# Performance work log

Hardware: AMD Instinct MI355X
Metric: run time of the kernel (lower is better)

Reference implementation:

```python
import jax, jax.numpy as jnp
import numpy as np

LN_EPS = 1e-5      # torch.nn.LayerNorm default
NORM_EPS = 1e-12   # torch F.normalize default


def _layernorm(x, gamma, beta):
    mu = jnp.mean(x, axis=-1, keepdims=True)
    var = jnp.mean(jnp.square(x - mu), axis=-1, keepdims=True)
    return (x - mu) * jax.lax.rsqrt(var + LN_EPS) * gamma + beta


def _l2norm(x):
    # normalize over last (embedding) axis, matching F.normalize(dim=1) on [B,E,1,N]
    n = jnp.sqrt(jnp.sum(jnp.square(x), axis=-1, keepdims=True))
    return x / jnp.maximum(n, NORM_EPS)


def setup_inputs() -> dict:
    key = jax.random.key(0)
    ks = jax.random.split(key, 4)
    B, N, C, E = 8, 4096, 768, 768
    x = jax.random.normal(ks[0], (B, N, C), dtype=jnp.float32)
    w_qkv = jax.random.normal(ks[1], (C, 3 * E), dtype=jnp.float32) * (1.0 / np.sqrt(C))
    w_proj = jax.random.normal(ks[2], (E, C), dtype=jnp.float32) * (1.0 / np.sqrt(E))
    ln_in_g = jnp.ones((C,), jnp.float32)
    ln_in_b = jnp.zeros((C,), jnp.float32)
    ln_out_g = jnp.ones((E,), jnp.float32)
    ln_out_b = jnp.zeros((E,), jnp.float32)
    return {"x": x, "w_qkv": w_qkv, "w_proj": w_proj,
            "ln_in_g": ln_in_g, "ln_in_b": ln_in_b,
            "ln_out_g": ln_out_g, "ln_out_b": ln_out_b}


def reference(x, w_qkv, w_proj, ln_in_g, ln_in_b, ln_out_g, ln_out_b):
    # x: [B, N, C]
    h = _layernorm(x, ln_in_g, ln_in_b)
    qkv = h @ w_qkv                                  # [B, N, 3E]
    q, k, v = jnp.split(qkv, 3, axis=-1)             # each [B, N, E]
    phi_q = _l2norm(q)                               # per-token L2 over E
    phi_k = _l2norm(k)
    kv = jnp.sum(phi_k * v, axis=1)                  # [B, E] (sum over tokens N)
    attn = phi_q * kv[:, None, :]                    # [B, N, E]
    out = _layernorm(attn, ln_out_g, ln_out_b) @ w_proj  # [B, N, C]
    return out
```

## Files before the change

### kernel.cpp

```cpp
#include <hip/hip_runtime.h>
#include <hip/hip_bf16.h>
#include <cstdint>

typedef __bf16 bf16;
typedef __bf16 bf16x4 __attribute__((ext_vector_type(4)));
typedef __bf16 bf16x8 __attribute__((ext_vector_type(8)));
typedef float f32x4 __attribute__((ext_vector_type(4)));

#define GK 768
#define LN_EPS 1e-5f
#define NORM_EPS 1e-12f

__device__ __forceinline__ void gl_lds16(const void* g, void* l) {
  __builtin_amdgcn_global_load_lds(
      (__attribute__((address_space(1))) uint32_t*)(uintptr_t)g,
      (__attribute__((address_space(3))) uint32_t*)(uintptr_t)l,
      16, 0, 0);
}

__device__ __forceinline__ void blockReduce2w3(float& s, float& ss, float* sm) {
  #pragma unroll
  for (int o = 32; o > 0; o >>= 1) {
    s  += __shfl_down(s, o, 64);
    ss += __shfl_down(ss, o, 64);
  }
  int wave = threadIdx.x >> 6, lane = threadIdx.x & 63;
  if (lane == 0) { sm[wave] = s; sm[3 + wave] = ss; }
  __syncthreads();
  s  = sm[0] + sm[1] + sm[2];
  ss = sm[3] + sm[4] + sm[5];
  __syncthreads();
}

__global__ __launch_bounds__(256) void transpose_cvt(const float* __restrict__ w,
                                                     bf16* __restrict__ wt,
                                                     int R, int Ncols) {
  __shared__ float tile[32][33];
  int tx = threadIdx.x & 31, ty = threadIdx.x >> 5;
  int c0 = blockIdx.x * 32, r0 = blockIdx.y * 32;
  #pragma unroll
  for (int i = 0; i < 32; i += 8)
    tile[ty + i][tx] = w[(size_t)(r0 + ty + i) * Ncols + (c0 + tx)];
  __syncthreads();
  #pragma unroll
  for (int i = 0; i < 32; i += 8)
    wt[(size_t)(c0 + ty + i) * R + (r0 + tx)] = (bf16)tile[tx][ty + i];
}

__global__ __launch_bounds__(192) void ln_in_kernel(const float* __restrict__ x,
                                                    const float* __restrict__ g,
                                                    const float* __restrict__ b,
                                                    bf16* __restrict__ h) {
  __shared__ float sm[6];
  int row = blockIdx.x, t = threadIdx.x;
  const float* xr = x + (size_t)row * 768;
  float4 v = ((const float4*)xr)[t];
  float s  = v.x + v.y + v.z + v.w;
  float ss = v.x * v.x + v.y * v.y + v.z * v.z + v.w * v.w;
  blockReduce2w3(s, ss, sm);
  float mu  = s * (1.0f / 768.0f);
  float inv = rsqrtf(ss * (1.0f / 768.0f) - mu * mu + LN_EPS);
  float4 gg = ((const float4*)g)[t];
  float4 bb = ((const float4*)b)[t];
  bf16x4 o;
  o[0] = (bf16)((v.x - mu) * inv * gg.x + bb.x);
  o[1] = (bf16)((v.y - mu) * inv * gg.y + bb.y);
  o[2] = (bf16)((v.z - mu) * inv * gg.z + bb.z);
  o[3] = (bf16)((v.w - mu) * inv * gg.w + bb.w);
  ((bf16x4*)(h + (size_t)row * 768))[t] = o;
}


#define SWZ(x) ((x) ^ ((((x) >> 7) & 7) << 4))

#define BAR __builtin_amdgcn_s_barrier()
#define VMC(n) asm volatile("s_waitcnt vmcnt(" #n ")" ::: "memory")
#define PRIO1 __builtin_amdgcn_s_setprio(1)
#define PRIO0 __builtin_amdgcn_s_setprio(0)

#define LDA1(base, i, ks) \
  af[i][ks] = *(const bf16x8*)((base) + SWZ((wm * 64 + (i) * 16 + llo) * 128 + (ks) * 64 + lhi * 16))
#define LDB1(base, j, ks) \
  bf[j][ks] = *(const bf16x8*)((base) + SWZ((wn * 64 + (j) * 16 + llo) * 128 + (ks) * 64 + lhi * 16))
#define RDALL(Ab, Bb) do { \
  LDA1(Ab, 0, 0); LDA1(Ab, 1, 0); LDA1(Ab, 2, 0); LDA1(Ab, 3, 0); \
  LDB1(Bb, 0, 0); LDB1(Bb, 1, 0); LDB1(Bb, 2, 0); LDB1(Bb, 3, 0); \
  LDA1(Ab, 0, 1); LDA1(Ab, 1, 1); LDA1(Ab, 2, 1); LDA1(Ab, 3, 1); \
  LDB1(Bb, 0, 1); LDB1(Bb, 1, 1); LDB1(Bb, 2, 1); LDB1(Bb, 3, 1); } while (0)

#define MF1(m, n, ks) \
  acc[m][n] = __builtin_amdgcn_mfma_f32_16x16x32_bf16(af[m][ks], bf[n][ks], acc[m][n], 0, 0, 0)
#define MFALL do { PRIO1; \
  MF1(0,0,0); MF1(0,1,0); MF1(0,2,0); MF1(0,3,0); \
  MF1(1,0,0); MF1(1,1,0); MF1(1,2,0); MF1(1,3,0); \
  MF1(2,0,0); MF1(2,1,0); MF1(2,2,0); MF1(2,3,0); \
  MF1(3,0,0); MF1(3,1,0); MF1(3,2,0); MF1(3,3,0); \
  MF1(0,0,1); MF1(0,1,1); MF1(0,2,1); MF1(0,3,1); \
  MF1(1,0,1); MF1(1,1,1); MF1(1,2,1); MF1(1,3,1); \
  MF1(2,0,1); MF1(2,1,1); MF1(2,2,1); MF1(2,3,1); \
  MF1(3,0,1); MF1(3,1,1); MF1(3,2,1); MF1(3,3,1); \
  PRIO0; } while (0)

#define STA2(b, q, t) gl_lds16(A + srcA[q] + (t) * 64, &As_[b][(q) * 2048 + wave * 512])
#define STB2(b, q, t) gl_lds16(Bt + srcB[q] + (t) * 64, &Bs_[b][(q) * 2048 + wave * 512])
#define STAGE(b, t) do { \
  STA2(b, 0, t); STA2(b, 1, t); STA2(b, 2, t); STA2(b, 3, t); \
  STB2(b, 0, t); STB2(b, 1, t); STB2(b, 2, t); STB2(b, 3, t); } while (0)

template <bool OUT_BF16>
__global__ __launch_bounds__(256, 2) void gemm128(const bf16* __restrict__ A,
                                                  const bf16* __restrict__ Bt,
                                                  void* __restrict__ Cv,
                                                  int Nn, int NBN) {
  __shared__ __align__(16) bf16 As_[2][8192];
  __shared__ __align__(16) bf16 Bs_[2][8192];
  const int tid = threadIdx.x;
  const int wave = tid >> 6, lane = tid & 63;
  const int llo = lane & 15, lhi = lane >> 4;
  const int wm = wave >> 1, wn = wave & 1;

  const int nwg = gridDim.x, bid = blockIdx.x;
  const int wg = (bid & 7) * (nwg >> 3) + (bid >> 3);
  const int rb = wg / NBN, cb = wg - rb * NBN;
  const int brow = rb * 128, bcol = cb * 128;

  uint32_t srcA[4], srcB[4];
  #pragma unroll
  for (int q = 0; q < 4; ++q) {
    int d = q * 4096 + tid * 16;
    int a = SWZ(d);
    int r = a >> 7, c = (a & 127) >> 1;
    srcA[q] = (uint32_t)(brow + r) * GK + c;
    srcB[q] = (uint32_t)(bcol + r) * GK + c;
  }

  f32x4 acc[4][4];
  #pragma unroll
  for (int m = 0; m < 4; ++m)
    #pragma unroll
    for (int n = 0; n < 4; ++n) acc[m][n] = (f32x4){0.f, 0.f, 0.f, 0.f};

  bf16x8 af[4][2], bf[4][2];
  const char* As0 = (const char*)&As_[0][0];
  const char* As1 = (const char*)&As_[1][0];
  const char* Bs0 = (const char*)&Bs_[0][0];
  const char* Bs1 = (const char*)&Bs_[1][0];

  STAGE(0, 0);
  STAGE(1, 1);
  VMC(8);
  BAR;

  #pragma unroll
  for (int j = 0; j < 5; ++j) {
    RDALL(As0, Bs0);
    MFALL;
    BAR;
    STAGE(0, 2 * j + 2);
    VMC(8);
    BAR;
    RDALL(As1, Bs1);
    MFALL;
    BAR;
    STAGE(1, 2 * j + 3);
    VMC(8);
    BAR;
  }
  RDALL(As0, Bs0);
  MFALL;
  BAR;
  VMC(0);
  BAR;
  RDALL(As1, Bs1);
  MFALL;

  #pragma unroll
  for (int m = 0; m < 4; ++m) {
    #pragma unroll
    for (int n = 0; n < 4; ++n) {
      int row = brow + wm * 64 + m * 16 + lhi * 4;
      int col = bcol + wn * 64 + n * 16 + llo;
      #pragma unroll
      for (int r2 = 0; r2 < 4; ++r2) {
        if (OUT_BF16)
          ((bf16*)Cv)[(size_t)(row + r2) * Nn + col] = (bf16)acc[m][n][r2];
        else
          ((float*)Cv)[(size_t)(row + r2) * Nn + col] = acc[m][n][r2];
      }
    }
  }
}

__global__ __launch_bounds__(256) void kv_partial(const bf16* __restrict__ qkv,
                                                  float* __restrict__ kvp) {
  __shared__ float sm[4][768];
  int b = blockIdx.x >> 5, chunk = blockIdx.x & 31;
  int wave = threadIdx.x >> 6, lane = threadIdx.x & 63;
  const bf16* base = qkv + ((size_t)(b * 4096 + chunk * 128 + wave * 32)) * 2304;
  float acc[3][4] = {};
  for (int i = 0; i < 32; ++i) {
    const bf16* kr = base + (size_t)i * 2304 + 768;
    const bf16* vr = kr + 768;
    bf16x4 k4[3], v4[3];
    #pragma unroll
    for (int c = 0; c < 3; ++c) {
      k4[c] = *(const bf16x4*)(kr + c * 256 + lane * 4);
      v4[c] = *(const bf16x4*)(vr + c * 256 + lane * 4);
    }
    float ssk = 0.f;
    #pragma unroll
    for (int c = 0; c < 3; ++c)
      #pragma unroll
      for (int j = 0; j < 4; ++j) { float kf = (float)k4[c][j]; ssk += kf * kf; }
    #pragma unroll
    for (int off = 32; off > 0; off >>= 1) ssk += __shfl_xor(ssk, off, 64);
    float wi = 1.0f / fmaxf(sqrtf(ssk), NORM_EPS);
    #pragma unroll
    for (int c = 0; c < 3; ++c)
      #pragma unroll
      for (int j = 0; j < 4; ++j)
        acc[c][j] += (float)k4[c][j] * (float)v4[c][j] * wi;
  }
  #pragma unroll
  for (int c = 0; c < 3; ++c)
    #pragma unroll
    for (int j = 0; j < 4; ++j)
      sm[wave][c * 256 + lane * 4 + j] = acc[c][j];
  __syncthreads();
  int t = threadIdx.x;
  #pragma unroll
  for (int c = 0; c < 3; ++c) {
    int e = c * 256 + t;
    kvp[(size_t)blockIdx.x * 768 + e] = sm[0][e] + sm[1][e] + sm[2][e] + sm[3][e];
  }
}

__global__ __launch_bounds__(256) void kv_reduce(const float* __restrict__ kvp,
                                                 float* __restrict__ kv) {
  int i = blockIdx.x * 256 + threadIdx.x;
  int b = i / 768, e = i - b * 768;
  float s = 0.f;
  #pragma unroll
  for (int c = 0; c < 32; ++c) s += kvp[(size_t)(b * 32 + c) * 768 + e];
  kv[i] = s;
}

__global__ __launch_bounds__(192) void attn_ln_kernel(const bf16* __restrict__ qkv,
                                                      const float* __restrict__ kv,
                                                      const float* __restrict__ g,
                                                      const float* __restrict__ b,
                                                      bf16* __restrict__ a) {
  __shared__ float sm[6];
  int row = blockIdx.x, t = threadIdx.x;
  int bt = row >> 12;
  const bf16* qr = qkv + (size_t)row * 2304;
  bf16x4 q4 = ((const bf16x4*)qr)[t];
  float q0 = (float)q4[0], q1 = (float)q4[1], q2 = (float)q4[2], q3 = (float)q4[3];
  float sq = q0 * q0 + q1 * q1 + q2 * q2 + q3 * q3, dummy = 0.f;
  blockReduce2w3(sq, dummy, sm);
  float iq = 1.0f / fmaxf(sqrtf(sq), NORM_EPS);
  float4 kv4 = ((const float4*)(kv + bt * 768))[t];
  float4 av;
  av.x = q0 * iq * kv4.x;
  av.y = q1 * iq * kv4.y;
  av.z = q2 * iq * kv4.z;
  av.w = q3 * iq * kv4.w;
  float s  = av.x + av.y + av.z + av.w;
  float ss = av.x * av.x + av.y * av.y + av.z * av.z + av.w * av.w;
  blockReduce2w3(s, ss, sm);
  float mu  = s * (1.0f / 768.0f);
  float inv = rsqrtf(ss * (1.0f / 768.0f) - mu * mu + LN_EPS);
  float4 gg = ((const float4*)g)[t];
  float4 bb = ((const float4*)b)[t];
  bf16x4 o;
  o[0] = (bf16)((av.x - mu) * inv * gg.x + bb.x);
  o[1] = (bf16)((av.y - mu) * inv * gg.y + bb.y);
  o[2] = (bf16)((av.z - mu) * inv * gg.z + bb.z);
  o[3] = (bf16)((av.w - mu) * inv * gg.w + bb.w);
  ((bf16x4*)(a + (size_t)row * 768))[t] = o;
}

extern "C" void kernel_launch(void* const* d_in, const int* in_sizes, int n_in,
                              void* d_out, int out_size, void* d_ws, size_t ws_size,
                              hipStream_t stream) {
  const float* x      = (const float*)d_in[0];
  const float* w_qkv  = (const float*)d_in[1];
  const float* w_proj = (const float*)d_in[2];
  const float* g_in   = (const float*)d_in[3];
  const float* b_in   = (const float*)d_in[4];
  const float* g_out  = (const float*)d_in[5];
  const float* b_out  = (const float*)d_in[6];

  char* ws = (char*)d_ws;
  bf16*  wqkvt  = (bf16*)(ws);
  bf16*  wprojt = (bf16*)(ws + 3538944);
  bf16*  h      = (bf16*)(ws + 4718592);
  bf16*  qkv    = (bf16*)(ws + 55050240);
  float* kvp    = (float*)(ws + 206045184);
  float* kv     = (float*)(ws + 206831616);

  transpose_cvt<<<dim3(2304 / 32, 768 / 32), 256, 0, stream>>>(w_qkv, wqkvt, 768, 2304);
  transpose_cvt<<<dim3(768 / 32, 768 / 32), 256, 0, stream>>>(w_proj, wprojt, 768, 768);
  ln_in_kernel<<<32768, 192, 0, stream>>>(x, g_in, b_in, h);
  gemm128<true><<<256 * 18, 256, 0, stream>>>(h, wqkvt, (void*)qkv, 2304, 18);
  kv_partial<<<256, 256, 0, stream>>>(qkv, kvp);
  kv_reduce<<<24, 256, 0, stream>>>(kvp, kv);
  attn_ln_kernel<<<32768, 192, 0, stream>>>(qkv, kv, g_out, b_out, h);
  gemm128<false><<<256 * 6, 256, 0, stream>>>(h, wprojt, d_out, 768, 6);
}
```

Before: 268.9 us.

## Prepack weights in MFMA fragment order and load B directly into registers

The weight transpose kernel now writes weights in a per-wave MFMA fragment layout. The GEMM then loads B fragments straight from global memory into registers, double-buffered one K-step ahead, instead of staging them through LDS. This halves LDS traffic and LDS footprint per block and drops the B staging loads. The cost is that B reads now rely on L2/global latency being hidden by the register prefetch, and register pressure rises with two B fragment buffers.

```diff
diff --git a/kernel.cpp b/kernel.cpp
--- a/kernel.cpp
+++ b/kernel.cpp
@@ -32,19 +32,28 @@
   __syncthreads();
 }
 
-__global__ __launch_bounds__(256) void transpose_cvt(const float* __restrict__ w,
-                                                     bf16* __restrict__ wt,
-                                                     int R, int Ncols) {
+__global__ __launch_bounds__(256) void transpose_cvt_pack(const float* __restrict__ w,
+                                                          bf16* __restrict__ pack,
+                                                          int Ncols) {
   __shared__ float tile[32][33];
   int tx = threadIdx.x & 31, ty = threadIdx.x >> 5;
-  int c0 = blockIdx.x * 32, r0 = blockIdx.y * 32;
+  int c0 = blockIdx.x * 32, k0 = blockIdx.y * 32;
   #pragma unroll
   for (int i = 0; i < 32; i += 8)
-    tile[ty + i][tx] = w[(size_t)(r0 + ty + i) * Ncols + (c0 + tx)];
+    tile[ty + i][tx] = w[(size_t)(k0 + ty + i) * Ncols + (c0 + tx)];
   __syncthreads();
-  #pragma unroll
-  for (int i = 0; i < 32; i += 8)
-    wt[(size_t)(c0 + ty + i) * R + (r0 + tx)] = (bf16)tile[tx][ty + i];
+  int tid = threadIdx.x;
+  if (tid < 128) {
+    int fi = tid >> 6, lane = tid & 63;
+    int llo = lane & 15, lhi = lane >> 4;
+    int cb = c0 >> 7, wn = (c0 >> 6) & 1, j = ((c0 & 63) >> 4) + fi;
+    int t = k0 >> 6, ks = (k0 >> 5) & 1;
+    int f = ((cb * 2 + wn) * 12 + t) * 8 + (j * 2 + ks);
+    bf16x8 o;
+    #pragma unroll
+    for (int e = 0; e < 8; ++e) o[e] = (bf16)tile[lhi * 8 + e][fi * 16 + llo];
+    *(bf16x8*)(pack + (size_t)f * 512 + lane * 8) = o;
+  }
 }
 
 __global__ __launch_bounds__(192) void ln_in_kernel(const float* __restrict__ x,
@@ -80,40 +89,38 @@
 
 #define LDA1(base, i, ks) \
   af[i][ks] = *(const bf16x8*)((base) + SWZ((wm * 64 + (i) * 16 + llo) * 128 + (ks) * 64 + lhi * 16))
-#define LDB1(base, j, ks) \
-  bf[j][ks] = *(const bf16x8*)((base) + SWZ((wn * 64 + (j) * 16 + llo) * 128 + (ks) * 64 + lhi * 16))
-#define RDALL(Ab, Bb) do { \
+#define RDALL_A(Ab) do { \
   LDA1(Ab, 0, 0); LDA1(Ab, 1, 0); LDA1(Ab, 2, 0); LDA1(Ab, 3, 0); \
-  LDB1(Bb, 0, 0); LDB1(Bb, 1, 0); LDB1(Bb, 2, 0); LDB1(Bb, 3, 0); \
-  LDA1(Ab, 0, 1); LDA1(Ab, 1, 1); LDA1(Ab, 2, 1); LDA1(Ab, 3, 1); \
-  LDB1(Bb, 0, 1); LDB1(Bb, 1, 1); LDB1(Bb, 2, 1); LDB1(Bb, 3, 1); } while (0)
-
-#define MF1(m, n, ks) \
-  acc[m][n] = __builtin_amdgcn_mfma_f32_16x16x32_bf16(af[m][ks], bf[n][ks], acc[m][n], 0, 0, 0)
-#define MFALL do { PRIO1; \
-  MF1(0,0,0); MF1(0,1,0); MF1(0,2,0); MF1(0,3,0); \
-  MF1(1,0,0); MF1(1,1,0); MF1(1,2,0); MF1(1,3,0); \
-  MF1(2,0,0); MF1(2,1,0); MF1(2,2,0); MF1(2,3,0); \
-  MF1(3,0,0); MF1(3,1,0); MF1(3,2,0); MF1(3,3,0); \
-  MF1(0,0,1); MF1(0,1,1); MF1(0,2,1); MF1(0,3,1); \
-  MF1(1,0,1); MF1(1,1,1); MF1(1,2,1); MF1(1,3,1); \
-  MF1(2,0,1); MF1(2,1,1); MF1(2,2,1); MF1(2,3,1); \
-  MF1(3,0,1); MF1(3,1,1); MF1(3,2,1); MF1(3,3,1); \
+  LDA1(Ab, 0, 1); LDA1(Ab, 1, 1); LDA1(Ab, 2, 1); LDA1(Ab, 3, 1); } while (0)
+
+#define BLOADP(S, P) do { \
+  S[0][0] = *(const bf16x8*)((P) + 0);    S[0][1] = *(const bf16x8*)((P) + 512); \
+  S[1][0] = *(const bf16x8*)((P) + 1024); S[1][1] = *(const bf16x8*)((P) + 1536); \
+  S[2][0] = *(const bf16x8*)((P) + 2048); S[2][1] = *(const bf16x8*)((P) + 2560); \
+  S[3][0] = *(const bf16x8*)((P) + 3072); S[3][1] = *(const bf16x8*)((P) + 3584); } while (0)
+
+#define MF1S(S, m, n, ks) \
+  acc[m][n] = __builtin_amdgcn_mfma_f32_16x16x32_bf16(af[m][ks], S[n][ks], acc[m][n], 0, 0, 0)
+#define MFALLS(S) do { PRIO1; \
+  MF1S(S,0,0,0); MF1S(S,0,1,0); MF1S(S,0,2,0); MF1S(S,0,3,0); \
+  MF1S(S,1,0,0); MF1S(S,1,1,0); MF1S(S,1,2,0); MF1S(S,1,3,0); \
+  MF1S(S,2,0,0); MF1S(S,2,1,0); MF1S(S,2,2,0); MF1S(S,2,3,0); \
+  MF1S(S,3,0,0); MF1S(S,3,1,0); MF1S(S,3,2,0); MF1S(S,3,3,0); \
+  MF1S(S,0,0,1); MF1S(S,0,1,1); MF1S(S,0,2,1); MF1S(S,0,3,1); \
+  MF1S(S,1,0,1); MF1S(S,1,1,1); MF1S(S,1,2,1); MF1S(S,1,3,1); \
+  MF1S(S,2,0,1); MF1S(S,2,1,1); MF1S(S,2,2,1); MF1S(S,2,3,1); \
+  MF1S(S,3,0,1); MF1S(S,3,1,1); MF1S(S,3,2,1); MF1S(S,3,3,1); \
   PRIO0; } while (0)
 
 #define STA2(b, q, t) gl_lds16(A + srcA[q] + (t) * 64, &As_[b][(q) * 2048 + wave * 512])
-#define STB2(b, q, t) gl_lds16(Bt + srcB[q] + (t) * 64, &Bs_[b][(q) * 2048 + wave * 512])
-#define STAGE(b, t) do { \
-  STA2(b, 0, t); STA2(b, 1, t); STA2(b, 2, t); STA2(b, 3, t); \
-  STB2(b, 0, t); STB2(b, 1, t); STB2(b, 2, t); STB2(b, 3, t); } while (0)
+#define STAGE(b, t) do { STA2(b, 0, t); STA2(b, 1, t); STA2(b, 2, t); STA2(b, 3, t); } while (0)
 
 template <bool OUT_BF16>
-__global__ __launch_bounds__(256, 2) void gemm128(const bf16* __restrict__ A,
-                                                  const bf16* __restrict__ Bt,
-                                                  void* __restrict__ Cv,
-                                                  int Nn, int NBN) {
+__global__ __launch_bounds__(256, 2) void gemm128b(const bf16* __restrict__ A,
+                                                   const bf16* __restrict__ Bp,
+                                                   void* __restrict__ Cv,
+                                                   int Nn, int NBN) {
   __shared__ __align__(16) bf16 As_[2][8192];
-  __shared__ __align__(16) bf16 Bs_[2][8192];
   const int tid = threadIdx.x;
   const int wave = tid >> 6, lane = tid & 63;
   const int llo = lane & 15, lhi = lane >> 4;
@@ -124,15 +131,16 @@
   const int rb = wg / NBN, cb = wg - rb * NBN;
   const int brow = rb * 128, bcol = cb * 128;
 
-  uint32_t srcA[4], srcB[4];
+  uint32_t srcA[4];
   #pragma unroll
   for (int q = 0; q < 4; ++q) {
     int d = q * 4096 + tid * 16;
     int a = SWZ(d);
     int r = a >> 7, c = (a & 127) >> 1;
     srcA[q] = (uint32_t)(brow + r) * GK + c;
-    srcB[q] = (uint32_t)(bcol + r) * GK + c;
-  }
+  }
+
+  const bf16* bp = Bp + (size_t)(cb * 2 + wn) * 49152 + lane * 8;
 
   f32x4 acc[4][4];
   #pragma unroll
@@ -140,39 +148,42 @@
     #pragma unroll
     for (int n = 0; n < 4; ++n) acc[m][n] = (f32x4){0.f, 0.f, 0.f, 0.f};
 
-  bf16x8 af[4][2], bf[4][2];
+  bf16x8 af[4][2], bfA[4][2], bfB[4][2];
   const char* As0 = (const char*)&As_[0][0];
   const char* As1 = (const char*)&As_[1][0];
-  const char* Bs0 = (const char*)&Bs_[0][0];
-  const char* Bs1 = (const char*)&Bs_[1][0];
-
+
+  BLOADP(bfA, bp);
   STAGE(0, 0);
   STAGE(1, 1);
-  VMC(8);
+
+  for (int jp = 0; jp < 5; ++jp) {
+    const int t = 2 * jp;
+    VMC(4);
+    BAR;
+    RDALL_A(As0);
+    BLOADP(bfB, bp + 4096);
+    MFALLS(bfA);
+    BAR;
+    STAGE(0, t + 2);
+    VMC(4);
+    BAR;
+    RDALL_A(As1);
+    BLOADP(bfA, bp + 8192);
+    MFALLS(bfB);
+    BAR;
+    STAGE(1, t + 3);
+    bp += 8192;
+  }
+  VMC(4);
   BAR;
-
-  #pragma unroll
-  for (int j = 0; j < 5; ++j) {
-    RDALL(As0, Bs0);
-    MFALL;
-    BAR;
-    STAGE(0, 2 * j + 2);
-    VMC(8);
-    BAR;
-    RDALL(As1, Bs1);
-    MFALL;
-    BAR;
-    STAGE(1, 2 * j + 3);
-    VMC(8);
-    BAR;
-  }
-  RDALL(As0, Bs0);
-  MFALL;
+  RDALL_A(As0);
+  BLOADP(bfB, bp + 4096);
+  MFALLS(bfA);
   BAR;
   VMC(0);
   BAR;
-  RDALL(As1, Bs1);
-  MFALL;
+  RDALL_A(As1);
+  MFALLS(bfB);
 
   #pragma unroll
   for (int m = 0; m < 4; ++m) {
@@ -292,19 +303,19 @@
   const float* b_out  = (const float*)d_in[6];
 
   char* ws = (char*)d_ws;
-  bf16*  wqkvt  = (bf16*)(ws);
-  bf16*  wprojt = (bf16*)(ws + 3538944);
+  bf16*  bqp    = (bf16*)(ws);
+  bf16*  bpp    = (bf16*)(ws + 3538944);
   bf16*  h      = (bf16*)(ws + 4718592);
   bf16*  qkv    = (bf16*)(ws + 55050240);
   float* kvp    = (float*)(ws + 206045184);
   float* kv     = (float*)(ws + 206831616);
 
-  transpose_cvt<<<dim3(2304 / 32, 768 / 32), 256, 0, stream>>>(w_qkv, wqkvt, 768, 2304);
-  transpose_cvt<<<dim3(768 / 32, 768 / 32), 256, 0, stream>>>(w_proj, wprojt, 768, 768);
+  transpose_cvt_pack<<<dim3(2304 / 32, 768 / 32), 256, 0, stream>>>(w_qkv, bqp, 2304);
+  transpose_cvt_pack<<<dim3(768 / 32, 768 / 32), 256, 0, stream>>>(w_proj, bpp, 768);
   ln_in_kernel<<<32768, 192, 0, stream>>>(x, g_in, b_in, h);
-  gemm128<true><<<256 * 18, 256, 0, stream>>>(h, wqkvt, (void*)qkv, 2304, 18);
+  gemm128b<true><<<256 * 18, 256, 0, stream>>>(h, bqp, (void*)qkv, 2304, 18);
   kv_partial<<<256, 256, 0, stream>>>(qkv, kvp);
   kv_reduce<<<24, 256, 0, stream>>>(kvp, kv);
   attn_ln_kernel<<<32768, 192, 0, stream>>>(qkv, kv, g_out, b_out, h);
-  gemm128<false><<<256 * 6, 256, 0, stream>>>(h, wprojt, d_out, 768, 6);
-}
+  gemm128b<false><<<256 * 6, 256, 0, stream>>>(h, bpp, d_out, 768, 6);
+}
```

Result: slower. 279.3 us (+3.9%).
